# Optimization experiments

Measured on AMD Instinct MI355X. Metric: run time of the kernel, lower is better.

The kernel has to match this reference:

```python
import jax, jax.numpy as jnp
import numpy as np

VOCAB_SIZE = 62  # string.ascii_letters + string.digits
HIDDEN = 1024
STATE = int(HIDDEN * 4.0)  # state_size_mult=4.0
B, L = 2, 2048


def setup_inputs() -> dict:
    key = jax.random.key(0)
    ks = jax.random.split(key, 6)
    g = lambda k, shape, scale: (jax.random.normal(k, shape, jnp.float32) * scale)
    return {
        "tokens": jax.random.randint(ks[0], (B, L), 0, VOCAB_SIZE),
        "embed_w": g(ks[1], (VOCAB_SIZE, HIDDEN), 1.0),
        "norm_w": jnp.ones((HIDDEN,), jnp.float32),
        "in_w": g(ks[2], (HIDDEN, 4 * STATE), HIDDEN ** -0.5),
        "in_b": jnp.zeros((4 * STATE,), jnp.float32),
        "out_w": g(ks[3], (STATE, HIDDEN), STATE ** -0.5),
        "out_b": jnp.zeros((HIDDEN,), jnp.float32),
        "head_w": g(ks[4], (HIDDEN, VOCAB_SIZE), HIDDEN ** -0.5),
        "head_b": jnp.zeros((VOCAB_SIZE,), jnp.float32),
    }


def _rmsnorm(x, w, eps=1e-6):
    var = jnp.mean(x * x, axis=-1, keepdims=True)
    return x * jax.lax.rsqrt(var + eps) * w


def reference(tokens, embed_w, norm_w, in_w, in_b, out_w, out_b, head_w, head_b):
    # embedding lookup: [B, L, H]
    x = embed_w[tokens]
    res = x
    xn = _rmsnorm(x, norm_w)
    # single fused projection to (x_inner, a, b, c), each [B, L, STATE]
    proj = xn @ in_w + in_b
    xg, a_l, b_l, c_l = jnp.split(proj, 4, axis=-1)
    a = jax.nn.sigmoid(a_l)            # forget gate in (0,1)
    bx = jax.nn.sigmoid(b_l) * xg      # input contribution b_t * x_t
    # linear recurrence h_t = a_t * h_{t-1} + b_t * x_t via associative scan
    def comb(e1, e2):
        a1, h1 = e1
        a2, h2 = e2
        return a1 * a2, a2 * h1 + h2
    _, h = jax.lax.associative_scan(comb, (a, bx), axis=1)
    y = jax.nn.sigmoid(c_l) * h        # output gate c_t * h_t
    out = y @ out_w + out_b + res      # project back to hidden + residual
    return out @ head_w + head_b       # vocab logits [B, L, 62]
```

## Files before the change

### kernel.cpp

```cpp
#include <hip/hip_runtime.h>
#include <math.h>

#define HID   1024
#define STT   4096
#define MTOK  4096
#define LSEQ  2048
#define NCHUNK 64
#define CHUNK  32
#define VOCAB  62

typedef __attribute__((ext_vector_type(8))) short short8v;
typedef __attribute__((ext_vector_type(4))) float float4v;

typedef const __attribute__((address_space(1))) void* gptr_t;
typedef __attribute__((address_space(3))) void* lptr_t;

__device__ __forceinline__ float sigmoidf_(float x) {
    return 1.0f / (1.0f + __expf(-x));
}
__device__ __forceinline__ unsigned short f2bf(float f) {
    unsigned int u = __float_as_uint(f);
    unsigned int r = (u + 0x7fffu + ((u >> 16) & 1u)) >> 16;
    return (unsigned short)r;
}
__device__ __forceinline__ float bf2f(unsigned short b) {
    return __uint_as_float(((unsigned int)b) << 16);
}

__global__ __launch_bounds__(256) void fused_pre(
    const int* __restrict__ tokens, const float* __restrict__ embed_w,
    const float* __restrict__ norm_w, const float* __restrict__ in_w,
    const float* __restrict__ out_w, const float* __restrict__ head_w,
    const float* __restrict__ out_b, const float* __restrict__ head_b,
    unsigned short* __restrict__ in_wT, unsigned short* __restrict__ xn,
    unsigned short* __restrict__ W2T, float* __restrict__ E_head)
{
    __shared__ float sh[1056];
    int bid = blockIdx.x;
    int tid = threadIdx.x;
    if (bid < 16384) {
        float (*tile)[33] = (float (*)[33])sh;
        int c0 = (bid & 511) * 32, r0 = (bid >> 9) * 32;
        int r = tid >> 3, c4 = (tid & 7) << 2;
        float4 v = *(const float4*)(in_w + (size_t)(r0 + r) * 16384 + c0 + c4);
        tile[r][c4 + 0] = v.x; tile[r][c4 + 1] = v.y;
        tile[r][c4 + 2] = v.z; tile[r][c4 + 3] = v.w;
        __syncthreads();
        int oc = tid >> 3;
        int orr = (tid & 7) << 2;
        ushort4 o;
        o.x = f2bf(tile[orr + 0][oc]); o.y = f2bf(tile[orr + 1][oc]);
        o.z = f2bf(tile[orr + 2][oc]); o.w = f2bf(tile[orr + 3][oc]);
        *(ushort4*)(in_wT + (size_t)(c0 + oc) * 1024 + r0 + orr) = o;
    } else if (bid < 20480) {
        int m = bid - 16384;
        int tok = tokens[m];
        float4 x = ((const float4*)(embed_w + (size_t)tok * HID))[tid];
        float ss = x.x * x.x + x.y * x.y + x.z * x.z + x.w * x.w;
        for (int off = 32; off > 0; off >>= 1) ss += __shfl_down(ss, off);
        if ((tid & 63) == 0) sh[tid >> 6] = ss;
        __syncthreads();
        float tot = sh[0] + sh[1] + sh[2] + sh[3];
        float scale = rsqrtf(tot / (float)HID + 1e-6f);
        float4 w4 = ((const float4*)norm_w)[tid];
        ushort4 o;
        o.x = f2bf(x.x * scale * w4.x); o.y = f2bf(x.y * scale * w4.y);
        o.z = f2bf(x.z * scale * w4.z); o.w = f2bf(x.w * scale * w4.w);
        *(ushort4*)(xn + (size_t)m * HID + (tid << 2)) = o;
    } else if (bid < 21504) {
        float (*red)[4][64] = (float (*)[4][64])sh;
        int jc = tid >> 6, n = tid & 63;
        bool act = n < VOCAB;
        int k0 = (bid - 20480) * 4;
        float a[4] = {0.f, 0.f, 0.f, 0.f};
        int j0 = jc * 256;
        const float* w0 = out_w + (size_t)(k0 + 0) * HID;
        const float* w1 = out_w + (size_t)(k0 + 1) * HID;
        const float* w2 = out_w + (size_t)(k0 + 2) * HID;
        const float* w3 = out_w + (size_t)(k0 + 3) * HID;
        #pragma unroll 4
        for (int j = j0; j < j0 + 256; j++) {
            float h = act ? head_w[(size_t)j * VOCAB + n] : 0.f;
            a[0] = fmaf(w0[j], h, a[0]);
            a[1] = fmaf(w1[j], h, a[1]);
            a[2] = fmaf(w2[j], h, a[2]);
            a[3] = fmaf(w3[j], h, a[3]);
        }
        #pragma unroll
        for (int i = 0; i < 4; i++) red[jc][i][n] = a[i];
        __syncthreads();
        if (jc == 0) {
            #pragma unroll
            for (int i = 0; i < 4; i++) {
                float s = red[0][i][n] + red[1][i][n] + red[2][i][n] + red[3][i][n];
                W2T[(size_t)n * STT + k0 + i] = f2bf(s);
            }
        }
    } else {
        float (*red)[4][64] = (float (*)[4][64])sh;
        int jc = tid >> 6, n = tid & 63;
        bool act = n < VOCAB;
        int t = bid - 21504;
        const float* src = (t < VOCAB) ? (embed_w + (size_t)t * HID) : out_b;
        float acc = 0.f;
        if (act) {
            int j0 = jc * 256;
            #pragma unroll 4
            for (int j = j0; j < j0 + 256; j++)
                acc = fmaf(src[j], head_w[(size_t)j * VOCAB + n], acc);
        }
        red[jc][0][n] = acc;
        __syncthreads();
        if (tid < 64) {
            float s = red[0][0][n] + red[1][0][n] + red[2][0][n] + red[3][0][n];
            if (t == VOCAB && act) s += head_b[n];
            E_head[t * 64 + n] = s;
        }
    }
}

__global__ __launch_bounds__(512, 2) void gemm_in_mfma(
    const unsigned short* __restrict__ A, const unsigned short* __restrict__ B,
    const float* __restrict__ bias,
    unsigned short* __restrict__ a_out, unsigned short* __restrict__ bx_out,
    unsigned short* __restrict__ c_out)
{
    extern __shared__ unsigned short lds[];
    int tid = threadIdx.x;
    int wid = tid >> 6, lane = tid & 63;
    int wg = blockIdx.x;
    int xcd = wg & 7, loc = wg >> 3;
    int by = ((xcd >> 1) << 2) + (loc & 3);
    int bx = ((xcd & 1) << 5) + (loc >> 2);
    int m0 = by * 256, s0 = bx * 64;
    int wm = wid >> 2, wn = wid & 3;
    int lr = lane & 15, lk = lane >> 4;

    int cb0 = wid * 64, cb1 = 512 + wid * 64;
    int p0 = cb0 + lane, p1 = cb1 + lane;
    int row0 = p0 >> 2, ks0 = (p0 & 3) ^ ((row0 >> 1) & 3);
    int row1 = p1 >> 2, ks1 = (p1 & 3) ^ ((row1 >> 1) & 3);
    int arow0 = m0 + row0, arow1 = m0 + row1;
    int brow0 = ((row0 >> 6) << 12) + s0 + (row0 & 63);
    int brow1 = ((row1 >> 6) << 12) + s0 + (row1 & 63);

#define SHALF(grow0, grow1, b, which, kt, kk) do {                               \
    unsigned short* _d = lds + (b) * 32768 + (which) * 16384 + (kk) * 8192;      \
    __builtin_amdgcn_global_load_lds(                                            \
        (gptr_t)(const void*)(((which) ? B : A) + (size_t)(grow0) * 1024 +       \
                              (kt) * 64 + (kk) * 32 + ks0 * 8),                  \
        (lptr_t)(void*)(_d + (size_t)cb0 * 8), 16, 0, 0);                        \
    __builtin_amdgcn_global_load_lds(                                            \
        (gptr_t)(const void*)(((which) ? B : A) + (size_t)(grow1) * 1024 +       \
                              (kt) * 64 + (kk) * 32 + ks1 * 8),                  \
        (lptr_t)(void*)(_d + (size_t)cb1 * 8), 16, 0, 0);                        \
} while (0)

    int ksw = lk ^ ((lr >> 1) & 3);

#define RD_A(b, kk, mf) \
    (*(const short8v*)&lds[(b) * 32768 + (kk) * 8192 + \
        (((wm * 128 + (mf) * 16 + lr) << 2) + ksw) * 8])
#define RD_B(b, kk, nf) \
    (*(const short8v*)&lds[(b) * 32768 + 16384 + (kk) * 8192 + \
        ((((nf) * 64 + wn * 16 + lr) << 2) + ksw) * 8])

#define MFMA8x2(AF, B0, B1, n0i, n1i) do {                                       \
    __builtin_amdgcn_s_setprio(1);                                               \
    _Pragma("unroll")                                                            \
    for (int mf = 0; mf < 8; mf++) {                                             \
        acc[mf][n0i] = __builtin_amdgcn_mfma_f32_16x16x32_bf16(                  \
            (AF)[mf], (B0), acc[mf][n0i], 0, 0, 0);                              \
        acc[mf][n1i] = __builtin_amdgcn_mfma_f32_16x16x32_bf16(                  \
            (AF)[mf], (B1), acc[mf][n1i], 0, 0, 0);                              \
    }                                                                            \
    __builtin_amdgcn_s_setprio(0);                                               \
} while (0)

#define BAR_IN()  do { __builtin_amdgcn_s_barrier();                              \
    asm volatile("s_waitcnt lgkmcnt(0)" ::: "memory");                           \
    __builtin_amdgcn_sched_barrier(0); } while (0)
#define BAR_OUT() do { asm volatile("" ::: "memory");                             \
    __builtin_amdgcn_s_barrier(); } while (0)

    float4v acc[8][4];
    float4v z = {0.f, 0.f, 0.f, 0.f};
    #pragma unroll
    for (int i = 0; i < 8; i++)
        #pragma unroll
        for (int j = 0; j < 4; j++) acc[i][j] = z;

    SHALF(arow0, arow1, 0, 0, 0, 0); SHALF(brow0, brow1, 0, 1, 0, 0);
    SHALF(arow0, arow1, 0, 0, 0, 1); SHALF(brow0, brow1, 0, 1, 0, 1);
    asm volatile("s_waitcnt vmcnt(0)" ::: "memory");
    __builtin_amdgcn_s_barrier();

    short8v af[8], bf0, bf1;

    for (int kt = 0; kt < 16; ++kt) {
        int cur = kt & 1, nxt = cur ^ 1;
        int ktn = kt < 15 ? kt + 1 : 15;
        #pragma unroll
        for (int mf = 0; mf < 8; mf++) af[mf] = RD_A(cur, 0, mf);
        bf0 = RD_B(cur, 0, 0); bf1 = RD_B(cur, 0, 1);
        asm volatile("s_waitcnt vmcnt(4)" ::: "memory");
        SHALF(arow0, arow1, nxt, 0, ktn, 0);
        BAR_IN();
        MFMA8x2(af, bf0, bf1, 0, 1);
        BAR_OUT();
        bf0 = RD_B(cur, 0, 2); bf1 = RD_B(cur, 0, 3);
        SHALF(brow0, brow1, nxt, 1, ktn, 0);
        BAR_IN();
        MFMA8x2(af, bf0, bf1, 2, 3);
        BAR_OUT();
        #pragma unroll
        for (int mf = 0; mf < 8; mf++) af[mf] = RD_A(cur, 1, mf);
        bf0 = RD_B(cur, 1, 0); bf1 = RD_B(cur, 1, 1);
        asm volatile("s_waitcnt vmcnt(4)" ::: "memory");
        SHALF(arow0, arow1, nxt, 0, ktn, 1);
        BAR_IN();
        MFMA8x2(af, bf0, bf1, 0, 1);
        BAR_OUT();
        bf0 = RD_B(cur, 1, 2); bf1 = RD_B(cur, 1, 3);
        SHALF(brow0, brow1, nxt, 1, ktn, 1);
        BAR_IN();
        MFMA8x2(af, bf0, bf1, 2, 3);
        BAR_OUT();
    }

    int s = s0 + wn * 16 + lr;
    float b_xg = bias[s];
    float b_a  = bias[4096 + s];
    float b_b  = bias[8192 + s];
    float b_c  = bias[12288 + s];
    int rbase = lk << 2;
    #pragma unroll
    for (int mf = 0; mf < 8; mf++)
        #pragma unroll
        for (int q = 0; q < 4; q++) {
            int m = m0 + wm * 128 + mf * 16 + rbase + q;
            size_t idx = (size_t)m * STT + s;
            float xg = acc[mf][0][q] + b_xg;
            float a  = sigmoidf_(acc[mf][1][q] + b_a);
            float bxv = sigmoidf_(acc[mf][2][q] + b_b) * xg;
            float c  = sigmoidf_(acc[mf][3][q] + b_c);
            a_out[idx]  = f2bf(a);
            bx_out[idx] = f2bf(bxv);
            c_out[idx]  = f2bf(c);
        }
#undef SHALF
#undef RD_A
#undef RD_B
#undef MFMA8x2
#undef BAR_IN
#undef BAR_OUT
}

__global__ __launch_bounds__(256, 3) void logits_gemm(
    const unsigned short* __restrict__ Y, const unsigned short* __restrict__ W2T,
    float* __restrict__ part)
{
    extern __shared__ unsigned short lds[];
    int tid = threadIdx.x;
    int wid = tid >> 6, lane = tid & 63;
    int wg = blockIdx.x;
    int m0 = (wg & 31) * 128;
    int slice = wg >> 5;
    int ks0 = slice * 512;
    int wm = wid >> 1, wn = wid & 1;
    int lr = lane & 15, lk = lane >> 4;

    auto stage = [&](int b, int kt) {
        unsigned short* As = lds + b * 6144;
        unsigned short* Bs = As + 4096;
        #pragma unroll
        for (int i = 0; i < 2; i++) {
            int cb = i * 256 + wid * 64;
            int p = cb + lane;
            int row = p >> 2;
            int ks = (p & 3) ^ ((row >> 1) & 3);
            __builtin_amdgcn_global_load_lds(
                (gptr_t)(const void*)(Y + (size_t)(m0 + row) * STT + kt + ks * 8),
                (lptr_t)(void*)(As + (size_t)cb * 8), 16, 0, 0);
        }
        {
            int cb = wid * 64;
            int p = cb + lane;
            int row = p >> 2;
            int ks = (p & 3) ^ ((row >> 1) & 3);
            __builtin_amdgcn_global_load_lds(
                (gptr_t)(const void*)(W2T + (size_t)row * STT + kt + ks * 8),
                (lptr_t)(void*)(Bs + (size_t)cb * 8), 16, 0, 0);
        }
    };

    float4v acc[4][2];
    float4v z = {0.f, 0.f, 0.f, 0.f};
    #pragma unroll
    for (int i = 0; i < 4; i++) { acc[i][0] = z; acc[i][1] = z; }

    const int nt = 16;
    stage(0, ks0); stage(1, ks0 + 32);

    int ksw = lk ^ ((lr >> 1) & 3);

    for (int t = 0; t < nt; ++t) {
        if (t + 2 < nt) stage((t + 2) % 3, ks0 + (t + 2) * 32);
        if (t + 2 < nt)      asm volatile("s_waitcnt vmcnt(6)" ::: "memory");
        else if (t + 1 < nt) asm volatile("s_waitcnt vmcnt(3)" ::: "memory");
        else                 asm volatile("s_waitcnt vmcnt(0)" ::: "memory");
        __builtin_amdgcn_s_barrier();
        asm volatile("" ::: "memory");
        const unsigned short* As = lds + (t % 3) * 6144;
        const unsigned short* Bs = As + 4096;
        short8v af[4], bfr[2];
        #pragma unroll
        for (int f = 0; f < 4; f++)
            af[f] = *(const short8v*)&As[(((wm * 64 + f * 16 + lr) << 2) + ksw) * 8];
        #pragma unroll
        for (int g = 0; g < 2; g++)
            bfr[g] = *(const short8v*)&Bs[(((wn * 32 + g * 16 + lr) << 2) + ksw) * 8];
        __builtin_amdgcn_s_setprio(1);
        #pragma unroll
        for (int f = 0; f < 4; f++)
            #pragma unroll
            for (int g = 0; g < 2; g++)
                acc[f][g] = __builtin_amdgcn_mfma_f32_16x16x32_bf16(
                    af[f], bfr[g], acc[f][g], 0, 0, 0);
        __builtin_amdgcn_s_setprio(0);
        asm volatile("" ::: "memory");
        __builtin_amdgcn_s_barrier();
    }

    float* pb = part + (size_t)slice * MTOK * 64;
    int rbase = lk << 2;
    #pragma unroll
    for (int f = 0; f < 4; f++)
        #pragma unroll
        for (int g = 0; g < 2; g++) {
            int n = wn * 32 + g * 16 + lr;
            #pragma unroll
            for (int q = 0; q < 4; q++) {
                int m = m0 + wm * 64 + f * 16 + rbase + q;
                pb[(size_t)m * 64 + n] = acc[f][g][q];
            }
        }
}

__global__ __launch_bounds__(64) void logits_reduce(
    const float* __restrict__ part, const float* __restrict__ E_head,
    const int* __restrict__ tokens, float* __restrict__ logits)
{
    int m = blockIdx.x;
    int n = threadIdx.x;
    if (n >= VOCAB) return;
    int tok = tokens[m];
    float s = E_head[tok * 64 + n] + E_head[VOCAB * 64 + n];
    #pragma unroll
    for (int sl = 0; sl < 8; sl++)
        s += part[(size_t)sl * MTOK * 64 + (size_t)m * 64 + n];
    logits[(size_t)m * VOCAB + n] = s;
}

__global__ __launch_bounds__(256) void scan_phase1(
    const unsigned short* __restrict__ a_buf, const unsigned short* __restrict__ bx_buf,
    float* __restrict__ chunkA, float* __restrict__ chunkH)
{
    int bid = blockIdx.x;
    int sg = bid & 3, q = (bid >> 2) & 63, b = bid >> 8;
    int s0 = sg * 1024 + threadIdx.x * 4;
    size_t base = (size_t)(b * LSEQ + q * CHUNK) * STT + s0;
    const unsigned short* ap = a_buf + base;
    const unsigned short* bp = bx_buf + base;
    float Aa[4] = {1.f, 1.f, 1.f, 1.f}, Hh[4] = {0.f, 0.f, 0.f, 0.f};
    for (int t = 0; t < CHUNK; t++) {
        ushort4 Av = *(const ushort4*)ap;
        ushort4 Bv = *(const ushort4*)bp;
        const unsigned short* avp = (const unsigned short*)&Av;
        const unsigned short* bvp = (const unsigned short*)&Bv;
        #pragma unroll
        for (int j = 0; j < 4; j++) {
            float a = bf2f(avp[j]);
            Hh[j] = fmaf(a, Hh[j], bf2f(bvp[j]));
            Aa[j] *= a;
        }
        ap += STT; bp += STT;
    }
    #pragma unroll
    for (int j = 0; j < 4; j++) {
        int ch = b * STT + s0 + j;
        chunkA[ch * NCHUNK + q] = Aa[j];
        chunkH[ch * NCHUNK + q] = Hh[j];
    }
}

__global__ __launch_bounds__(256) void scan_phase2(
    const float* __restrict__ chunkA, const float* __restrict__ chunkH,
    float* __restrict__ carry)
{
    int ch = blockIdx.x * 256 + threadIdx.x;
    float c = 0.f;
    for (int q = 0; q < NCHUNK; q++) {
        carry[ch * NCHUNK + q] = c;
        c = fmaf(chunkA[ch * NCHUNK + q], c, chunkH[ch * NCHUNK + q]);
    }
}

__global__ __launch_bounds__(256) void scan_phase3(
    const unsigned short* __restrict__ a_buf, const unsigned short* __restrict__ bx_buf,
    const unsigned short* __restrict__ c_buf, const float* __restrict__ carry,
    unsigned short* __restrict__ y)
{
    int bid = blockIdx.x;
    int sg = bid & 3, q = (bid >> 2) & 63, b = bid >> 8;
    int s0 = sg * 1024 + threadIdx.x * 4;
    float h[4];
    #pragma unroll
    for (int j = 0; j < 4; j++)
        h[j] = carry[(b * STT + s0 + j) * NCHUNK + q];
    size_t base = (size_t)(b * LSEQ + q * CHUNK) * STT + s0;
    const unsigned short* ap = a_buf + base;
    const unsigned short* bp = bx_buf + base;
    const unsigned short* cp = c_buf + base;
    unsigned short* yp = y + base;
    for (int t = 0; t < CHUNK; t++) {
        ushort4 Av = *(const ushort4*)ap;
        ushort4 Bv = *(const ushort4*)bp;
        ushort4 Cv = *(const ushort4*)cp;
        const unsigned short* avp = (const unsigned short*)&Av;
        const unsigned short* bvp = (const unsigned short*)&Bv;
        const unsigned short* cvp = (const unsigned short*)&Cv;
        ushort4 o;
        unsigned short* op = (unsigned short*)&o;
        #pragma unroll
        for (int j = 0; j < 4; j++) {
            h[j] = fmaf(bf2f(avp[j]), h[j], bf2f(bvp[j]));
            op[j] = f2bf(bf2f(cvp[j]) * h[j]);
        }
        *(ushort4*)yp = o;
        ap += STT; bp += STT; cp += STT; yp += STT;
    }
}

extern "C" void kernel_launch(void* const* d_in, const int* in_sizes, int n_in,
                              void* d_out, int out_size, void* d_ws, size_t ws_size,
                              hipStream_t stream) {
    const int*   tokens  = (const int*)d_in[0];
    const float* embed_w = (const float*)d_in[1];
    const float* norm_w  = (const float*)d_in[2];
    const float* in_w    = (const float*)d_in[3];
    const float* in_b    = (const float*)d_in[4];
    const float* out_w   = (const float*)d_in[5];
    const float* out_b   = (const float*)d_in[6];
    const float* head_w  = (const float*)d_in[7];
    const float* head_b  = (const float*)d_in[8];
    float* logits = (float*)d_out;

    char* w = (char*)d_ws;
    unsigned short* a_buf  = (unsigned short*)w;
    unsigned short* bx_buf = (unsigned short*)(w + 33554432);
    unsigned short* c_buf  = (unsigned short*)(w + 67108864);
    unsigned short* W2T    = (unsigned short*)(w + 100663296);
    float*          E_head = (float*)(w + 101711872);
    float*          part   = (float*)(w + 102760448);
    unsigned short* y      = (unsigned short*)(w + 134217728);
    unsigned short* in_wT  = (unsigned short*)(w + 167772160);
    unsigned short* xn     = (unsigned short*)(w + 201326592);
    float* chunkA = (float*)(w + 209715200);
    float* chunkH = chunkA + 8192 * NCHUNK;
    float* carry  = chunkH + 8192 * NCHUNK;

    hipLaunchKernelGGL(fused_pre, dim3(16384 + 4096 + 1024 + VOCAB + 1), dim3(256), 0, stream,
                       tokens, embed_w, norm_w, in_w, out_w, head_w, out_b, head_b,
                       in_wT, xn, W2T, E_head);
    hipLaunchKernelGGL(gemm_in_mfma, dim3(1024), dim3(512), 131072, stream,
                       xn, in_wT, in_b, a_buf, bx_buf, c_buf);
    hipLaunchKernelGGL(scan_phase1, dim3(512), dim3(256), 0, stream,
                       a_buf, bx_buf, chunkA, chunkH);
    hipLaunchKernelGGL(scan_phase2, dim3(32), dim3(256), 0, stream,
                       chunkA, chunkH, carry);
    hipLaunchKernelGGL(scan_phase3, dim3(512), dim3(256), 0, stream,
                       a_buf, bx_buf, c_buf, carry, y);
    hipLaunchKernelGGL(logits_gemm, dim3(256), dim3(256), 36864, stream,
                       y, W2T, part);
    hipLaunchKernelGGL(logits_reduce, dim3(MTOK), dim3(64), 0, stream,
                       part, E_head, tokens, logits);
}
```

Baseline: 288.3 us.

## Fuse chunk-level scan summaries into input GEMM epilogue, drop scan_phase1

The input-projection GEMM epilogue now computes each 32-step chunk's (A,H) recurrence summary directly from its accumulator registers, combining lane groups with shuffles and fragment pairs. The separate scan_phase1 kernel, which re-read the a and bx buffers from global memory, is removed. This saves one launch and 64 MB of bf16 reads, at the cost of extra shuffle and ALU work plus register pressure in the GEMM epilogue. It uses the bf16-rounded values so results match the old path.

```diff
diff --git a/kernel.cpp b/kernel.cpp
--- a/kernel.cpp
+++ b/kernel.cpp
@@ -123,7 +123,8 @@
     const unsigned short* __restrict__ A, const unsigned short* __restrict__ B,
     const float* __restrict__ bias,
     unsigned short* __restrict__ a_out, unsigned short* __restrict__ bx_out,
-    unsigned short* __restrict__ c_out)
+    unsigned short* __restrict__ c_out,
+    float* __restrict__ chunkA, float* __restrict__ chunkH)
 {
     extern __shared__ unsigned short lds[];
     int tid = threadIdx.x;
@@ -234,20 +235,49 @@
     float b_b  = bias[8192 + s];
     float b_c  = bias[12288 + s];
     int rbase = lk << 2;
-    #pragma unroll
-    for (int mf = 0; mf < 8; mf++)
-        #pragma unroll
-        for (int q = 0; q < 4; q++) {
-            int m = m0 + wm * 128 + mf * 16 + rbase + q;
-            size_t idx = (size_t)m * STT + s;
-            float xg = acc[mf][0][q] + b_xg;
-            float a  = sigmoidf_(acc[mf][1][q] + b_a);
-            float bxv = sigmoidf_(acc[mf][2][q] + b_b) * xg;
-            float c  = sigmoidf_(acc[mf][3][q] + b_c);
-            a_out[idx]  = f2bf(a);
-            bx_out[idx] = f2bf(bxv);
-            c_out[idx]  = f2bf(c);
-        }
+    int bb = m0 >> 11;
+    int t0 = m0 & 2047;
+    int ch = bb * STT + s;
+
+    #pragma unroll
+    for (int cc = 0; cc < 4; cc++) {
+        float Afr[2], Hfr[2];
+        #pragma unroll
+        for (int e = 0; e < 2; e++) {
+            int mf = cc * 2 + e;
+            float Al = 1.f, Hl = 0.f;
+            #pragma unroll
+            for (int q = 0; q < 4; q++) {
+                int m = m0 + wm * 128 + mf * 16 + rbase + q;
+                size_t idx = (size_t)m * STT + s;
+                float xg = acc[mf][0][q] + b_xg;
+                float av = sigmoidf_(acc[mf][1][q] + b_a);
+                float bxv = sigmoidf_(acc[mf][2][q] + b_b) * xg;
+                float cv = sigmoidf_(acc[mf][3][q] + b_c);
+                unsigned short au = f2bf(av), bu = f2bf(bxv);
+                a_out[idx]  = au;
+                bx_out[idx] = bu;
+                c_out[idx]  = f2bf(cv);
+                float ar = bf2f(au), br = bf2f(bu);
+                Hl = fmaf(ar, Hl, br);
+                Al = ar * Al;
+            }
+            #pragma unroll
+            for (int d = 1; d <= 2; d <<= 1) {
+                float Ap = __shfl(Al, lane - (d << 4));
+                float Hp = __shfl(Hl, lane - (d << 4));
+                if (lk >= d) { Hl = fmaf(Al, Hp, Hl); Al = Al * Ap; }
+            }
+            Afr[e] = Al; Hfr[e] = Hl;
+        }
+        if (lk == 3) {
+            float Ac = Afr[1] * Afr[0];
+            float Hc = fmaf(Afr[1], Hfr[0], Hfr[1]);
+            int qg = (t0 >> 5) + wm * 4 + cc;
+            chunkA[ch * NCHUNK + qg] = Ac;
+            chunkH[ch * NCHUNK + qg] = Hc;
+        }
+    }
 #undef SHALF
 #undef RD_A
 #undef RD_B
@@ -360,38 +390,6 @@
     for (int sl = 0; sl < 8; sl++)
         s += part[(size_t)sl * MTOK * 64 + (size_t)m * 64 + n];
     logits[(size_t)m * VOCAB + n] = s;
-}
-
-__global__ __launch_bounds__(256) void scan_phase1(
-    const unsigned short* __restrict__ a_buf, const unsigned short* __restrict__ bx_buf,
-    float* __restrict__ chunkA, float* __restrict__ chunkH)
-{
-    int bid = blockIdx.x;
-    int sg = bid & 3, q = (bid >> 2) & 63, b = bid >> 8;
-    int s0 = sg * 1024 + threadIdx.x * 4;
-    size_t base = (size_t)(b * LSEQ + q * CHUNK) * STT + s0;
-    const unsigned short* ap = a_buf + base;
-    const unsigned short* bp = bx_buf + base;
-    float Aa[4] = {1.f, 1.f, 1.f, 1.f}, Hh[4] = {0.f, 0.f, 0.f, 0.f};
-    for (int t = 0; t < CHUNK; t++) {
-        ushort4 Av = *(const ushort4*)ap;
-        ushort4 Bv = *(const ushort4*)bp;
-        const unsigned short* avp = (const unsigned short*)&Av;
-        const unsigned short* bvp = (const unsigned short*)&Bv;
-        #pragma unroll
-        for (int j = 0; j < 4; j++) {
-            float a = bf2f(avp[j]);
-            Hh[j] = fmaf(a, Hh[j], bf2f(bvp[j]));
-            Aa[j] *= a;
-        }
-        ap += STT; bp += STT;
-    }
-    #pragma unroll
-    for (int j = 0; j < 4; j++) {
-        int ch = b * STT + s0 + j;
-        chunkA[ch * NCHUNK + q] = Aa[j];
-        chunkH[ch * NCHUNK + q] = Hh[j];
-    }
 }
 
 __global__ __launch_bounds__(256) void scan_phase2(
@@ -474,9 +472,7 @@
                        tokens, embed_w, norm_w, in_w, out_w, head_w, out_b, head_b,
                        in_wT, xn, W2T, E_head);
     hipLaunchKernelGGL(gemm_in_mfma, dim3(1024), dim3(512), 131072, stream,
-                       xn, in_wT, in_b, a_buf, bx_buf, c_buf);
-    hipLaunchKernelGGL(scan_phase1, dim3(512), dim3(256), 0, stream,
-                       a_buf, bx_buf, chunkA, chunkH);
+                       xn, in_wT, in_b, a_buf, bx_buf, c_buf, chunkA, chunkH);
     hipLaunchKernelGGL(scan_phase2, dim3(32), dim3(256), 0, stream,
                        chunkA, chunkH, carry);
     hipLaunchKernelGGL(scan_phase3, dim3(512), dim3(256), 0, stream,
```

New measurement: 276.5 us. 1.04x faster.
